# Performance work log

Hardware: AMD Instinct MI355X
Metric: run time of the kernel (lower is better)

Reference implementation:

```python
import jax, jax.numpy as jnp
import numpy as np

N, B, FIN, E, EDIM, H, C = 20000, 2, 256, 320000, 64, 8, 32


def setup_inputs() -> dict:
    key = jax.random.key(0)
    ks = jax.random.split(key, 12)
    s = 1.0 / np.sqrt(FIN)
    se = 1.0 / np.sqrt(EDIM)
    return {
        "x": jax.random.normal(ks[0], (N, B, FIN), jnp.float32),
        "edata": jax.random.normal(ks[1], (E, EDIM), jnp.float32),
        "edge_src": jax.random.randint(ks[2], (E,), 0, N, jnp.int32),
        "edge_dst": jax.random.randint(ks[3], (E,), 0, N, jnp.int32),
        "Wq": jax.random.normal(ks[4], (FIN, H * C), jnp.float32) * s,
        "bq": jnp.zeros((H * C,), jnp.float32),
        "Wk": jax.random.normal(ks[5], (FIN, H * C), jnp.float32) * s,
        "bk": jnp.zeros((H * C,), jnp.float32),
        "Wv": jax.random.normal(ks[6], (FIN, H * C), jnp.float32) * s,
        "bv": jnp.zeros((H * C,), jnp.float32),
        "We": jax.random.normal(ks[7], (EDIM, H * C), jnp.float32) * se,
        "Wr": jax.random.normal(ks[8], (FIN, H * C), jnp.float32) * s,
        "br": jnp.zeros((H * C,), jnp.float32),
    }


def reference(x, edata, edge_src, edge_dst, Wq, bq, Wk, bk, Wv, bv, We, Wr, br):
    # x: [N, B, FIN]; edata: [E, EDIM]
    q = (x @ Wq + bq).reshape(N, B, H, C)   # dst queries
    k = (x @ Wk + bk).reshape(N, B, H, C)   # src keys
    v = (x @ Wv + bv).reshape(N, B, H, C)   # src values
    e = (edata @ We).reshape(E, 1, H, C)    # edge feats, broadcast over batch

    scale = 1.0 / np.sqrt(C)
    # per-edge logits: (u_mul_v / sqrt(C) + edata).sum(-1) -> [E, B, H]
    logits = (k[edge_src] * q[edge_dst] * scale + e).sum(-1)

    # edge_softmax over edges sharing the same destination node
    m = jax.ops.segment_max(logits, edge_dst, num_segments=N)      # [N, B, H]
    ex = jnp.exp(logits - m[edge_dst])
    z = jax.ops.segment_sum(ex, edge_dst, num_segments=N)          # [N, B, H]
    alpha = ex / z[edge_dst]                                       # [E, B, H]

    # weighted scatter-sum aggregation: u_mul_e + sum over dst
    att_v = v[edge_src] * alpha[..., None]                         # [E, B, H, C]
    agg = jax.ops.segment_sum(att_v, edge_dst, num_segments=N)     # [N, B, H, C]

    out = agg.reshape(N, B, H * C) + (x @ Wr + br)
    return out
```

## Files before the change

### kernel.cpp

```cpp
#include <hip/hip_runtime.h>
#include <hip/hip_bf16.h>

#define NN    20000
#define BB    2
#define EE    320000
#define MROWS (NN * BB)

typedef __bf16 bf16x8 __attribute__((ext_vector_type(8)));
typedef __bf16 bf16x4 __attribute__((ext_vector_type(4)));
typedef float  floatx4 __attribute__((ext_vector_type(4)));


#define NB_HIST 1250
#define NB_CVT  1250

__global__ __launch_bounds__(256) void prep_kernel(
    const float* __restrict__ Wq, const float* __restrict__ Wk,
    const float* __restrict__ Wv, const float* __restrict__ Wr,
    __hip_bfloat16* __restrict__ wt,
    const float* __restrict__ bq, const float* __restrict__ bk,
    const float* __restrict__ bv, const float* __restrict__ br,
    float* __restrict__ bcat,
    const float* __restrict__ We, float* __restrict__ wesum,
    const int* __restrict__ edst, int* __restrict__ counts,
    const float* __restrict__ x, __bf16* __restrict__ xb) {
  __shared__ float TA[32][65];
  __shared__ float TB[32][65];
  int bt = blockIdx.x;
  int t = threadIdx.x;

  if (bt < 16) {
    const float *A, *B;
    int c0, jbase;
    if (bt < 8) { A = Wk; B = Wv; c0 = 32 * bt;      jbase = 64 * bt; }
    else        { A = Wq; B = Wr; c0 = 32 * (bt-8);  jbase = 512 + 64 * (bt-8); }
    int krow = t >> 2;
    int cc = (t & 3) * 8;
    int sel = t >> 7;
    int u = t & 127;
    int ci = u >> 2;
    int kk0 = (u & 3) * 16;

    for (int kt = 0; kt < 4; ++kt) {
      int k = kt * 64 + krow;
      float4 a0 = *(const float4*)(A + (size_t)k * 256 + c0 + cc);
      float4 a1 = *(const float4*)(A + (size_t)k * 256 + c0 + cc + 4);
      float4 b0 = *(const float4*)(B + (size_t)k * 256 + c0 + cc);
      float4 b1 = *(const float4*)(B + (size_t)k * 256 + c0 + cc + 4);
      __syncthreads();
      TA[cc+0][krow]=a0.x; TA[cc+1][krow]=a0.y; TA[cc+2][krow]=a0.z; TA[cc+3][krow]=a0.w;
      TA[cc+4][krow]=a1.x; TA[cc+5][krow]=a1.y; TA[cc+6][krow]=a1.z; TA[cc+7][krow]=a1.w;
      TB[cc+0][krow]=b0.x; TB[cc+1][krow]=b0.y; TB[cc+2][krow]=b0.z; TB[cc+3][krow]=b0.w;
      TB[cc+4][krow]=b1.x; TB[cc+5][krow]=b1.y; TB[cc+6][krow]=b1.z; TB[cc+7][krow]=b1.w;
      __syncthreads();
      float (*T)[65] = sel ? TB : TA;
      int j = jbase + 2 * ci + sel;
      __hip_bfloat16* dst = wt + (size_t)j * 256 + kt * 64 + kk0;
      #pragma unroll
      for (int q = 0; q < 16; ++q) dst[q] = __float2bfloat16(T[ci][kk0 + q]);
    }
  } else if (bt == 16) {
    #pragma unroll
    for (int jj = 0; jj < 4; ++jj) {
      int j = jj * 256 + t;
      float val;
      if (j < 512) { int c = j >> 1;         val = (j & 1) ? bv[c] : bk[c]; }
      else         { int c = (j - 512) >> 1; val = (j & 1) ? br[c] : bq[c]; }
      bcat[j] = val;
    }
    #pragma unroll
    for (int ii = 0; ii < 2; ++ii) {
      int i = ii * 256 + t;
      int h = i >> 6, d = i & 63;
      float s = 0.f;
      for (int c = 0; c < 32; ++c) s += We[(size_t)d * 256 + h * 32 + c];
      wesum[h * 64 + d] = s;
    }
  } else if (bt < 17 + NB_HIST) {
    int e = (bt - 17) * 256 + t;
    if (e < EE) atomicAdd(&counts[edst[e]], 1);
  } else {
    int cb = bt - 17 - NB_HIST;
    size_t base = (size_t)cb * 8192 + t * 4;
    #pragma unroll
    for (int j = 0; j < 8; ++j) {
      float4 v = *(const float4*)(x + base + j * 1024);
      bf16x4 o;
      o[0] = (__bf16)v.x; o[1] = (__bf16)v.y;
      o[2] = (__bf16)v.z; o[3] = (__bf16)v.w;
      *(bf16x4*)(xb + base + j * 1024) = o;
    }
  }
}

__global__ void scan_kernel(const int* __restrict__ counts,
                            int* __restrict__ offsets,
                            int* __restrict__ cursor) {
  __shared__ int part[256];
  int t = threadIdx.x;
  const int per = (NN + 255) / 256;
  int lo = t * per, hi = min(lo + per, NN);
  int s = 0;
  #pragma unroll 4
  for (int i = lo; i < hi; ++i) s += counts[i];
  part[t] = s;
  __syncthreads();
  for (int off = 1; off < 256; off <<= 1) {
    int v = (t >= off) ? part[t - off] : 0;
    __syncthreads();
    part[t] += v;
    __syncthreads();
  }
  int base = (t == 0) ? 0 : part[t - 1];
  for (int i = lo; i < hi; ++i) {
    offsets[i] = base;
    cursor[i] = base;
    base += counts[i];
  }
  if (t == 255) offsets[NN] = base;
}

__global__ __launch_bounds__(256) void scatter_esum(
    const int* __restrict__ edst, const int* __restrict__ esrc,
    int* __restrict__ cursor,
    const float* __restrict__ edata, const float* __restrict__ wesum,
    int* __restrict__ ssrc, float* __restrict__ esum) {
  __shared__ float wl[512];
  int t = threadIdx.x;
  wl[t] = wesum[t];
  wl[t + 256] = wesum[t + 256];
  __syncthreads();
  int e = blockIdx.x * 256 + t;
  int p = atomicAdd(&cursor[edst[e]], 1);
  ssrc[p] = esrc[e];
  float acc[8] = {};
  const float* row = edata + (size_t)e * 64;
  for (int d = 0; d < 64; d += 4) {
    float4 v = *(const float4*)(row + d);
    #pragma unroll
    for (int hh = 0; hh < 8; ++hh) {
      const float* wv = &wl[hh * 64 + d];
      acc[hh] += v.x * wv[0] + v.y * wv[1] + v.z * wv[2] + v.w * wv[3];
    }
  }
  float* op = esum + (size_t)p * 8;
  *(float4*)op       = make_float4(acc[0], acc[1], acc[2], acc[3]);
  *(float4*)(op + 4) = make_float4(acc[4], acc[5], acc[6], acc[7]);
}

__global__ __launch_bounds__(256) void gemm_qkvr(
    const __bf16* __restrict__ xb,
    const __bf16* __restrict__ wt,
    const float* __restrict__ bcat,
    __hip_bfloat16* __restrict__ out) {
  const int LSTR = 72;
  __shared__ __attribute__((aligned(16))) __bf16 As[64 * LSTR];
  __shared__ __attribute__((aligned(16))) __bf16 Bs[256 * LSTR];

  int m0 = blockIdx.y * 64;
  int n0 = blockIdx.x * 256;
  int t = threadIdx.x;
  int w = t >> 6, l = t & 63;
  int lr = l & 15, lq = l >> 4;
  int ar = t >> 2, ac = (t & 3) * 16;

  floatx4 acc[4][4] = {};

  for (int ks = 0; ks < 4; ++ks) {
    const __bf16* xp = xb + (size_t)(m0 + ar) * 256 + ks * 64 + ac;
    bf16x8 a0 = *(const bf16x8*)xp;
    bf16x8 a1 = *(const bf16x8*)(xp + 8);
    const __bf16* wp = wt + (size_t)(n0 + t) * 256 + ks * 64;
    bf16x8 b0 = *(const bf16x8*)(wp);
    bf16x8 b1 = *(const bf16x8*)(wp + 8);
    bf16x8 b2 = *(const bf16x8*)(wp + 16);
    bf16x8 b3 = *(const bf16x8*)(wp + 24);
    bf16x8 b4 = *(const bf16x8*)(wp + 32);
    bf16x8 b5 = *(const bf16x8*)(wp + 40);
    bf16x8 b6 = *(const bf16x8*)(wp + 48);
    bf16x8 b7 = *(const bf16x8*)(wp + 56);
    __syncthreads();
    *(bf16x8*)&As[ar * LSTR + ac]     = a0;
    *(bf16x8*)&As[ar * LSTR + ac + 8] = a1;
    __bf16* bsr = &Bs[t * LSTR];
    *(bf16x8*)(bsr)      = b0;
    *(bf16x8*)(bsr + 8)  = b1;
    *(bf16x8*)(bsr + 16) = b2;
    *(bf16x8*)(bsr + 24) = b3;
    *(bf16x8*)(bsr + 32) = b4;
    *(bf16x8*)(bsr + 40) = b5;
    *(bf16x8*)(bsr + 48) = b6;
    *(bf16x8*)(bsr + 56) = b7;
    __syncthreads();
    #pragma unroll
    for (int kk = 0; kk < 2; ++kk) {
      bf16x8 af[4], bf_[4];
      #pragma unroll
      for (int mt = 0; mt < 4; ++mt)
        af[mt] = *(const bf16x8*)&As[(16 * mt + lr) * LSTR + kk * 32 + lq * 8];
      #pragma unroll
      for (int nt = 0; nt < 4; ++nt)
        bf_[nt] = *(const bf16x8*)&Bs[(64 * w + 16 * nt + lr) * LSTR + kk * 32 + lq * 8];
      #pragma unroll
      for (int mt = 0; mt < 4; ++mt)
        #pragma unroll
        for (int nt = 0; nt < 4; ++nt)
          acc[mt][nt] = __builtin_amdgcn_mfma_f32_16x16x32_bf16(af[mt], bf_[nt], acc[mt][nt], 0, 0, 0);
    }
  }

  #pragma unroll
  for (int mt = 0; mt < 4; ++mt)
    #pragma unroll
    for (int nt = 0; nt < 4; ++nt)
      #pragma unroll
      for (int r = 0; r < 4; ++r) {
        int gr = m0 + 16 * mt + lq * 4 + r;
        int gc = n0 + 64 * w + 16 * nt + lr;
        out[(size_t)gr * 1024 + gc] = __float2bfloat16(acc[mt][nt][r] + bcat[gc]);
      }
}

#define LOADSLOT(KV, EV, IDX)                                        \
  { int s_ = __builtin_amdgcn_readlane(s_l, (IDX));                  \
    KV = *(const uint4*)(kvl + (size_t)s_ * 1024);                   \
    EV = esp[(size_t)(IDX) * 8]; }

#define CONSUME(KV, EV)                                              \
  { float part = __uint_as_float(KV.x << 16) * q0                    \
               + __uint_as_float(KV.y << 16) * q1                    \
               + __uint_as_float(KV.z << 16) * q2                    \
               + __uint_as_float(KV.w << 16) * q3;                   \
    part += __shfl_xor(part, 1, 64);                                 \
    part += __shfl_xor(part, 2, 64);                                 \
    part += __shfl_xor(part, 4, 64);                                 \
    float p = __expf(part * 0.17677669529663687f + EV);              \
    z += p;                                                          \
    a0 += p * __uint_as_float(KV.x & 0xFFFF0000u);                   \
    a1 += p * __uint_as_float(KV.y & 0xFFFF0000u);                   \
    a2 += p * __uint_as_float(KV.z & 0xFFFF0000u);                   \
    a3 += p * __uint_as_float(KV.w & 0xFFFF0000u); }

__global__ __launch_bounds__(256) void aggregate_kernel(
    const unsigned int* __restrict__ qkvr,
    const float* __restrict__ esum,
    const int* __restrict__ offsets,
    const int* __restrict__ ssrc,
    float* __restrict__ out) {
  int t = threadIdx.x;
  int w = t >> 6, l = t & 63;
  int nb = blockIdx.x * 4 + w;
  int b = nb & 1, n = nb >> 1;
  int h = l >> 3;
  int beg = offsets[n], end = offsets[n + 1];

  uint4 qr4 = *(const uint4*)(qkvr + (size_t)nb * 512 + 256 + l * 4);
  float q0 = __uint_as_float(qr4.x << 16), q1 = __uint_as_float(qr4.y << 16);
  float q2 = __uint_as_float(qr4.z << 16), q3 = __uint_as_float(qr4.w << 16);

  const unsigned* kvl = qkvr + (size_t)b * 512 + l * 4;

  float z = 0.f, a0 = 0.f, a1 = 0.f, a2 = 0.f, a3 = 0.f;

  for (int base = beg; base < end; base += 64) {
    int chunk = min(64, end - base);
    int s_l = (l < chunk) ? ssrc[base + l] : 0;
    const float* esp = esum + (size_t)base * 8 + h;
    uint4 k0 = {0,0,0,0}, k1 = {0,0,0,0}, k2 = {0,0,0,0};
    uint4 k3 = {0,0,0,0}, k4 = {0,0,0,0}, k5 = {0,0,0,0};
    float e0 = 0.f, e1 = 0.f, e2 = 0.f, e3 = 0.f, e4 = 0.f, e5 = 0.f;
    LOADSLOT(k0, e0, 0);
    if (chunk > 1) LOADSLOT(k1, e1, 1);
    if (chunk > 2) LOADSLOT(k2, e2, 2);
    if (chunk > 3) LOADSLOT(k3, e3, 3);
    if (chunk > 4) LOADSLOT(k4, e4, 4);
    if (chunk > 5) LOADSLOT(k5, e5, 5);
    for (int i = 0; i < chunk; i += 6) {
      CONSUME(k0, e0);
      if (i + 6 < chunk) LOADSLOT(k0, e0, i + 6);
      if (i + 1 < chunk) {
        CONSUME(k1, e1);
        if (i + 7 < chunk) LOADSLOT(k1, e1, i + 7);
        if (i + 2 < chunk) {
          CONSUME(k2, e2);
          if (i + 8 < chunk) LOADSLOT(k2, e2, i + 8);
          if (i + 3 < chunk) {
            CONSUME(k3, e3);
            if (i + 9 < chunk) LOADSLOT(k3, e3, i + 9);
            if (i + 4 < chunk) {
              CONSUME(k4, e4);
              if (i + 10 < chunk) LOADSLOT(k4, e4, i + 10);
              if (i + 5 < chunk) {
                CONSUME(k5, e5);
                if (i + 11 < chunk) LOADSLOT(k5, e5, i + 11);
              }
            }
          }
        }
      }
    }
  }
  float inv = (z > 0.f) ? (1.0f / z) : 0.f;
  float4 o = make_float4(a0 * inv + __uint_as_float(qr4.x & 0xFFFF0000u),
                         a1 * inv + __uint_as_float(qr4.y & 0xFFFF0000u),
                         a2 * inv + __uint_as_float(qr4.z & 0xFFFF0000u),
                         a3 * inv + __uint_as_float(qr4.w & 0xFFFF0000u));
  *(float4*)(out + (size_t)nb * 256 + l * 4) = o;
}

extern "C" void kernel_launch(void* const* d_in, const int* in_sizes, int n_in,
                              void* d_out, int out_size, void* d_ws, size_t ws_size,
                              hipStream_t stream) {
  (void)in_sizes; (void)n_in; (void)out_size; (void)ws_size;
  const float* x     = (const float*)d_in[0];
  const float* edata = (const float*)d_in[1];
  const int* esrc    = (const int*)d_in[2];
  const int* edst    = (const int*)d_in[3];
  const float* Wq    = (const float*)d_in[4];
  const float* bq    = (const float*)d_in[5];
  const float* Wk    = (const float*)d_in[6];
  const float* bk    = (const float*)d_in[7];
  const float* Wv    = (const float*)d_in[8];
  const float* bv    = (const float*)d_in[9];
  const float* We    = (const float*)d_in[10];
  const float* Wr    = (const float*)d_in[11];
  const float* br    = (const float*)d_in[12];
  float* out = (float*)d_out;

  char* ws = (char*)d_ws;
  size_t off = 0;
  auto carve = [&](size_t bytes) -> void* {
    void* p = ws + off;
    off += (bytes + 255) & ~(size_t)255;
    return p;
  };
  int* counts    = (int*)carve((size_t)NN * 4);
  int* offsets   = (int*)carve((size_t)(NN + 1) * 4);
  int* cursor    = (int*)carve((size_t)NN * 4);
  int* ssrc      = (int*)carve((size_t)EE * 4);
  __hip_bfloat16* wt = (__hip_bfloat16*)carve((size_t)1024 * 256 * 2);
  float* bcat    = (float*)carve(1024 * 4);
  float* wesum   = (float*)carve(8 * 64 * 4);
  float* esum    = (float*)carve((size_t)EE * 8 * 4);
  __bf16* xb     = (__bf16*)carve((size_t)MROWS * 256 * 2);
  __hip_bfloat16* qkvr = (__hip_bfloat16*)carve((size_t)MROWS * 1024 * 2);

  hipMemsetAsync(counts, 0, (size_t)NN * 4, stream);
  prep_kernel<<<17 + NB_HIST + NB_CVT, 256, 0, stream>>>(
      Wq, Wk, Wv, Wr, wt, bq, bk, bv, br, bcat, We, wesum, edst, counts, x, xb);
  scan_kernel<<<1, 256, 0, stream>>>(counts, offsets, cursor);
  scatter_esum<<<EE / 256, 256, 0, stream>>>(edst, esrc, cursor, edata, wesum,
                                             ssrc, esum);
  gemm_qkvr<<<dim3(4, 625), 256, 0, stream>>>(xb, (const __bf16*)wt, bcat, qkvr);
  aggregate_kernel<<<MROWS / 4, 256, 0, stream>>>((const unsigned int*)qkvr, esum,
                                                  offsets, ssrc, out);
}
```

Measured before the change: 416.8 us.

## Load GEMM weight fragments directly from global and stage scan counts in LDS

The QKVR GEMM no longer stages the weight tile through shared memory. Each wave loads its B fragments straight from global memory into registers, which frees about 36KB of LDS per block and removes the LDS write/read traffic for B. The scan kernel now loads counts into LDS with coalesced reads, computes per-thread chunks there, and writes offsets back coalesced, replacing the strided global accesses. The trade-off is that B fragments are loaded redundantly from global memory (or L2) by each block instead of once into LDS, and the scan needs about 80KB of LDS in a single block.

```diff
diff --git a/kernel.cpp b/kernel.cpp
--- a/kernel.cpp
+++ b/kernel.cpp
@@ -93,16 +93,23 @@
   }
 }
 
-__global__ void scan_kernel(const int* __restrict__ counts,
-                            int* __restrict__ offsets,
-                            int* __restrict__ cursor) {
+#define SCAN_PAD (79 * 256)
+__global__ __launch_bounds__(256) void scan_kernel(
+    const int* __restrict__ counts,
+    int* __restrict__ offsets,
+    int* __restrict__ cursor) {
+  __shared__ int lc[SCAN_PAD];
   __shared__ int part[256];
   int t = threadIdx.x;
-  const int per = (NN + 255) / 256;
-  int lo = t * per, hi = min(lo + per, NN);
+  for (int j = 0; j < 79; ++j) {
+    int idx = j * 256 + t;
+    lc[idx] = (idx < NN) ? counts[idx] : 0;
+  }
+  __syncthreads();
+  int lo = t * 79;
   int s = 0;
   #pragma unroll 4
-  for (int i = lo; i < hi; ++i) s += counts[i];
+  for (int i = 0; i < 79; ++i) s += lc[lo + i];
   part[t] = s;
   __syncthreads();
   for (int off = 1; off < 256; off <<= 1) {
@@ -112,12 +119,21 @@
     __syncthreads();
   }
   int base = (t == 0) ? 0 : part[t - 1];
-  for (int i = lo; i < hi; ++i) {
-    offsets[i] = base;
-    cursor[i] = base;
-    base += counts[i];
+  for (int i = 0; i < 79; ++i) {
+    int c = lc[lo + i];
+    lc[lo + i] = base;
+    base += c;
   }
   if (t == 255) offsets[NN] = base;
+  __syncthreads();
+  for (int j = 0; j < 79; ++j) {
+    int idx = j * 256 + t;
+    if (idx < NN) {
+      int v = lc[idx];
+      offsets[idx] = v;
+      cursor[idx]  = v;
+    }
+  }
 }
 
 __global__ __launch_bounds__(256) void scatter_esum(
@@ -155,7 +171,6 @@
     __hip_bfloat16* __restrict__ out) {
   const int LSTR = 72;
   __shared__ __attribute__((aligned(16))) __bf16 As[64 * LSTR];
-  __shared__ __attribute__((aligned(16))) __bf16 Bs[256 * LSTR];
 
   int m0 = blockIdx.y * 64;
   int n0 = blockIdx.x * 256;
@@ -165,47 +180,33 @@
   int ar = t >> 2, ac = (t & 3) * 16;
 
   floatx4 acc[4][4] = {};
+  const __bf16* wbase = wt + (size_t)(n0 + 64 * w + lr) * 256 + lq * 8;
 
   for (int ks = 0; ks < 4; ++ks) {
     const __bf16* xp = xb + (size_t)(m0 + ar) * 256 + ks * 64 + ac;
     bf16x8 a0 = *(const bf16x8*)xp;
     bf16x8 a1 = *(const bf16x8*)(xp + 8);
-    const __bf16* wp = wt + (size_t)(n0 + t) * 256 + ks * 64;
-    bf16x8 b0 = *(const bf16x8*)(wp);
-    bf16x8 b1 = *(const bf16x8*)(wp + 8);
-    bf16x8 b2 = *(const bf16x8*)(wp + 16);
-    bf16x8 b3 = *(const bf16x8*)(wp + 24);
-    bf16x8 b4 = *(const bf16x8*)(wp + 32);
-    bf16x8 b5 = *(const bf16x8*)(wp + 40);
-    bf16x8 b6 = *(const bf16x8*)(wp + 48);
-    bf16x8 b7 = *(const bf16x8*)(wp + 56);
+    bf16x8 bfr[2][4];
+    #pragma unroll
+    for (int kk = 0; kk < 2; ++kk)
+      #pragma unroll
+      for (int nt = 0; nt < 4; ++nt)
+        bfr[kk][nt] = *(const bf16x8*)(wbase + (size_t)nt * 16 * 256 + ks * 64 + kk * 32);
     __syncthreads();
     *(bf16x8*)&As[ar * LSTR + ac]     = a0;
     *(bf16x8*)&As[ar * LSTR + ac + 8] = a1;
-    __bf16* bsr = &Bs[t * LSTR];
-    *(bf16x8*)(bsr)      = b0;
-    *(bf16x8*)(bsr + 8)  = b1;
-    *(bf16x8*)(bsr + 16) = b2;
-    *(bf16x8*)(bsr + 24) = b3;
-    *(bf16x8*)(bsr + 32) = b4;
-    *(bf16x8*)(bsr + 40) = b5;
-    *(bf16x8*)(bsr + 48) = b6;
-    *(bf16x8*)(bsr + 56) = b7;
     __syncthreads();
     #pragma unroll
     for (int kk = 0; kk < 2; ++kk) {
-      bf16x8 af[4], bf_[4];
+      bf16x8 af[4];
       #pragma unroll
       for (int mt = 0; mt < 4; ++mt)
         af[mt] = *(const bf16x8*)&As[(16 * mt + lr) * LSTR + kk * 32 + lq * 8];
-      #pragma unroll
-      for (int nt = 0; nt < 4; ++nt)
-        bf_[nt] = *(const bf16x8*)&Bs[(64 * w + 16 * nt + lr) * LSTR + kk * 32 + lq * 8];
       #pragma unroll
       for (int mt = 0; mt < 4; ++mt)
         #pragma unroll
         for (int nt = 0; nt < 4; ++nt)
-          acc[mt][nt] = __builtin_amdgcn_mfma_f32_16x16x32_bf16(af[mt], bf_[nt], acc[mt][nt], 0, 0, 0);
+          acc[mt][nt] = __builtin_amdgcn_mfma_f32_16x16x32_bf16(af[mt], bfr[kk][nt], acc[mt][nt], 0, 0, 0);
     }
   }
 
```

Result: faster. 382.1 us (-8.3%).
